# Optimization experiments

Measured on AMD Instinct MI355X. Metric: run time of the kernel, lower is better.

## Reference

```python
import jax, jax.numpy as jnp
import numpy as np

B, D_IN, H1, H2, LAT, K = 32768, 512, 256, 128, 64, 2048
BN_EPS = 1e-5
COMMIT = 0.25


def _linear_w(k, i, o):
    # xavier-uniform-ish init
    lim = np.sqrt(6.0 / (i + o)).astype(np.float32)
    return jax.random.uniform(k, (i, o), jnp.float32, -lim, lim)


def _bn_params(keys, n):
    g = jax.random.uniform(keys[0], (n,), jnp.float32, 0.5, 1.5)
    b = 0.1 * jax.random.normal(keys[1], (n,), jnp.float32)
    m = 0.1 * jax.random.normal(keys[2], (n,), jnp.float32)
    v = jax.random.uniform(keys[3], (n,), jnp.float32, 0.5, 1.5)
    return g, b, m, v


def setup_inputs() -> dict:
    key = jax.random.key(0)
    ks = jax.random.split(key, 32)
    inp = {"x": jax.random.normal(ks[0], (B, D_IN), jnp.float32)}
    # encoder: 512 -> 256 -> 128 -> 64
    inp["ew1"], inp["eb1"] = _linear_w(ks[1], D_IN, H1), jnp.zeros((H1,), jnp.float32)
    inp["eg1"], inp["ebt1"], inp["em1"], inp["ev1"] = _bn_params(jax.random.split(ks[2], 4), H1)
    inp["ew2"], inp["eb2"] = _linear_w(ks[3], H1, H2), jnp.zeros((H2,), jnp.float32)
    inp["eg2"], inp["ebt2"], inp["em2"], inp["ev2"] = _bn_params(jax.random.split(ks[4], 4), H2)
    inp["ew3"], inp["eb3"] = _linear_w(ks[5], H2, LAT), jnp.zeros((LAT,), jnp.float32)
    # codebook (num_embeddings, latent_dim)
    inp["codebook"] = _linear_w(ks[6], K, LAT).reshape(K, LAT)
    # decoder: 64 -> 128 -> 256 -> 512
    inp["dw1"], inp["db1"] = _linear_w(ks[7], LAT, H2), jnp.zeros((H2,), jnp.float32)
    inp["dg1"], inp["dbt1"], inp["dm1"], inp["dv1"] = _bn_params(jax.random.split(ks[8], 4), H2)
    inp["dw2"], inp["db2"] = _linear_w(ks[9], H2, H1), jnp.zeros((H1,), jnp.float32)
    inp["dg2"], inp["dbt2"], inp["dm2"], inp["dv2"] = _bn_params(jax.random.split(ks[10], 4), H1)
    inp["dw3"], inp["db3"] = _linear_w(ks[11], H1, D_IN), jnp.zeros((D_IN,), jnp.float32)
    return inp


def _bn(x, g, b, m, v):
    # BatchNorm1d in eval mode: running stats
    return (x - m) * (g * jax.lax.rsqrt(v + BN_EPS)) + b


def reference(x, ew1, eb1, eg1, ebt1, em1, ev1,
              ew2, eb2, eg2, ebt2, em2, ev2,
              ew3, eb3, codebook,
              dw1, db1, dg1, dbt1, dm1, dv1,
              dw2, db2, dg2, dbt2, dm2, dv2,
              dw3, db3):
    # ---- encoder MLP (Dropout is identity in eval) ----
    h = _bn(jax.nn.relu(x @ ew1 + eb1), eg1, ebt1, em1, ev1)
    h = _bn(jax.nn.relu(h @ ew2 + eb2), eg2, ebt2, em2, ev2)
    z_e = h @ ew3 + eb3  # [B, LAT]

    # ---- vector quantization: cdist + argmin + gather ----
    # squared L2 distance (argmin-equivalent to cdist p=2)
    d2 = (jnp.sum(z_e * z_e, axis=1, keepdims=True)
          + jnp.sum(codebook * codebook, axis=1)[None, :]
          - 2.0 * (z_e @ codebook.T))  # [B, K]
    idx = jnp.argmin(d2, axis=-1)  # [B]
    z_q = codebook[idx]  # gather, [B, LAT]

    codebook_loss = jnp.mean((z_q - jax.lax.stop_gradient(z_e)) ** 2)
    commit_loss = jnp.mean((z_e - jax.lax.stop_gradient(z_q)) ** 2)
    vq_loss = codebook_loss + COMMIT * commit_loss

    # straight-through estimator
    z_q = z_e + jax.lax.stop_gradient(z_q - z_e)

    # ---- decoder MLP ----
    h = _bn(jax.nn.relu(z_q @ dw1 + db1), dg1, dbt1, dm1, dv1)
    h = _bn(jax.nn.relu(h @ dw2 + db2), dg2, dbt2, dm2, dv2)
    x_recon = h @ dw3 + db3  # [B, D_IN]

    recon_err = jnp.mean((x_recon - x) ** 2)
    return x_recon, vq_loss, idx, recon_err
```

## Files before the change

### kernel.cpp

```cpp
#include <hip/hip_runtime.h>

#define B_ROWS 32768
#define D_IN   512
#define H1_N   256
#define H2_N   128
#define LAT_N  64
#define K_CB   2048

#define VQ_MARGIN 6.0e-3f
#define BK 32
#define BN 128

typedef __attribute__((ext_vector_type(8))) short s8v;
typedef __attribute__((ext_vector_type(4))) float f4v;

__device__ inline unsigned short f2bf(float f) {
    union { float f; unsigned u; } v; v.f = f;
    unsigned r = v.u + 0x7fffu + ((v.u >> 16) & 1u);
    return (unsigned short)(r >> 16);
}
__device__ inline float bf2f(unsigned short h) {
    union { unsigned u; float f; } v; v.u = ((unsigned)h) << 16;
    return v.f;
}

__device__ inline int pidx(int r, int k, int K) {
    return ((r >> 4) * (K >> 5) + (k >> 5)) * 512 + (((k >> 3) & 3) << 7)
         + ((r & 15) << 3) + (k & 7);
}

#define SWZ(row) ((((row) >> 2) & 7) << 3)

template <int MODE, int K, int CT, bool ASPLIT>
__global__ __launch_bounds__(256, 2) void mfma_gemm(
    const float* __restrict__ A_f32,
    const unsigned short* __restrict__ A_hi,
    const unsigned short* __restrict__ A_lo,
    const unsigned short* __restrict__ w_hi,
    const unsigned short* __restrict__ w_lo,
    const float* __restrict__ bias,
    const float* __restrict__ bn_g, const float* __restrict__ bn_b,
    const float* __restrict__ bn_m, const float* __restrict__ bn_v,
    unsigned short* __restrict__ out_hi, unsigned short* __restrict__ out_lo,
    float* __restrict__ out_f32,
    const float* __restrict__ xref, float* __restrict__ partials, int N)
{
    const int lane = threadIdx.x & 63;
    const int wv = threadIdx.x >> 6;
    const int wr = wv >> 1, wc = wv & 1;
    const int rbase = blockIdx.x * 128 + wr * 64;
    const int cbase = blockIdx.y * (32 * CT) + wc * (16 * CT);
    const int lr = lane & 15, lg = lane >> 4;

    f4v acc[4][CT];
#pragma unroll
    for (int rt = 0; rt < 4; ++rt)
#pragma unroll
        for (int ct = 0; ct < CT; ++ct)
            acc[rt][ct] = (f4v){0.f, 0.f, 0.f, 0.f};

    for (int ks = 0; ks < K / 32; ++ks) {
        s8v ah[4], al[4], bh[CT], bl[CT];
#pragma unroll
        for (int rt = 0; rt < 4; ++rt) {
            if constexpr (ASPLIT) {
                size_t aoff = (size_t)(rbase + rt * 16 + lr) * K + ks * 32 + lg * 8;
                const float* p = &A_f32[aoff];
                float4 v0 = *reinterpret_cast<const float4*>(p);
                float4 v1 = *reinterpret_cast<const float4*>(p + 4);
                float fv[8] = {v0.x, v0.y, v0.z, v0.w, v1.x, v1.y, v1.z, v1.w};
                unsigned uu[8], llv[8];
#pragma unroll
                for (int j = 0; j < 8; ++j) {
                    uu[j] = __float_as_uint(fv[j]);
                    float lo = fv[j] - __uint_as_float(uu[j] & 0xffff0000u);
                    llv[j] = __float_as_uint(lo);
                }
                union { s8v v; unsigned w[4]; } H, L;
#pragma unroll
                for (int m = 0; m < 4; ++m) {
                    H.w[m] = __builtin_amdgcn_perm(uu[2 * m + 1], uu[2 * m], 0x07060302u);
                    L.w[m] = __builtin_amdgcn_perm(llv[2 * m + 1], llv[2 * m], 0x07060302u);
                }
                ah[rt] = H.v;
                al[rt] = L.v;
            } else {
                int off = (((rbase >> 4) + rt) * (K >> 5) + ks) * 512 + lg * 128 + lr * 8;
                ah[rt] = *reinterpret_cast<const s8v*>(&A_hi[off]);
                al[rt] = *reinterpret_cast<const s8v*>(&A_lo[off]);
            }
        }
#pragma unroll
        for (int ct = 0; ct < CT; ++ct) {
            int off = (((cbase >> 4) + ct) * (K >> 5) + ks) * 512 + lg * 128 + lr * 8;
            bh[ct] = *reinterpret_cast<const s8v*>(&w_hi[off]);
            bl[ct] = *reinterpret_cast<const s8v*>(&w_lo[off]);
        }
#pragma unroll
        for (int rt = 0; rt < 4; ++rt)
#pragma unroll
            for (int ct = 0; ct < CT; ++ct) {
                acc[rt][ct] = __builtin_amdgcn_mfma_f32_16x16x32_bf16(
                    ah[rt], bh[ct], acc[rt][ct], 0, 0, 0);
                acc[rt][ct] = __builtin_amdgcn_mfma_f32_16x16x32_bf16(
                    al[rt], bh[ct], acc[rt][ct], 0, 0, 0);
                acc[rt][ct] = __builtin_amdgcn_mfma_f32_16x16x32_bf16(
                    ah[rt], bl[ct], acc[rt][ct], 0, 0, 0);
            }
    }

    float sq = 0.f;
#pragma unroll
    for (int ct = 0; ct < CT; ++ct) {
        int col = cbase + ct * 16 + lr;
        float bi = bias[col];
        float sc = 0.f, sh = 0.f;
        if (MODE == 0) {
            float s = bn_g[col] * rsqrtf(bn_v[col] + 1e-5f);
            sc = s;
            sh = bn_b[col] - bn_m[col] * s;
        }
#pragma unroll
        for (int rt = 0; rt < 4; ++rt)
#pragma unroll
            for (int i = 0; i < 4; ++i) {
                int row = rbase + rt * 16 + lg * 4 + i;
                float v = acc[rt][ct][i] + bi;
                if (MODE == 0) v = fmaxf(v, 0.f) * sc + sh;
                if (MODE == 0 || MODE == 3) {
                    unsigned u = __float_as_uint(v);
                    int p = pidx(row, col, N);
                    out_hi[p] = (unsigned short)(u >> 16);
                    out_lo[p] = f2bf(v - __uint_as_float(u & 0xffff0000u));
                }
                if (MODE == 2) {
                    float d = v - xref[(size_t)row * N + col];
                    sq = fmaf(d, d, sq);
                }
                if (MODE == 2 || MODE == 3)
                    out_f32[(size_t)row * N + col] = v;
            }
    }
    if (MODE == 2) {
        __shared__ float red[256];
        red[threadIdx.x] = sq;
        __syncthreads();
        for (int off = 128; off > 0; off >>= 1) {
            if (threadIdx.x < off) red[threadIdx.x] += red[threadIdx.x + off];
            __syncthreads();
        }
        if (threadIdx.x == 0)
            partials[blockIdx.y * gridDim.x + blockIdx.x] = red[0];
    }
}

template <int MODE, bool GATHER>
__global__ __launch_bounds__(256, 6) void rgemm(
    const int* __restrict__ rcnt, const int* __restrict__ rlist,
    const float* __restrict__ A, const float* __restrict__ W,
    const float* __restrict__ bias,
    const float* __restrict__ bn_g, const float* __restrict__ bn_b,
    const float* __restrict__ bn_m, const float* __restrict__ bn_v,
    float* __restrict__ out, int M, int N)
{
    const int count = min(rcnt[0], B_ROWS);
    const int row0 = blockIdx.x * 64;
    if (row0 >= count) return;
    __shared__ float sA[BK][64];
    __shared__ float sB[BK][BN];
    const int tid = threadIdx.x;
    const int tr = tid >> 4;
    const int tc = tid & 15;
    const int n0 = blockIdx.y * BN;

    float acc[4][8];
#pragma unroll
    for (int i = 0; i < 4; ++i)
#pragma unroll
        for (int j = 0; j < 8; ++j) acc[i][j] = 0.f;

    for (int k0 = 0; k0 < M; k0 += BK) {
#pragma unroll
        for (int it = 0; it < 2; ++it) {
            int s = tid + it * 256;
            int m = s >> 3;
            int kq = s & 7;
            int i = row0 + m;
            int src;
            if (GATHER) {
                int rr = (i < count) ? rlist[i] : 0;
                src = ((unsigned)rr < (unsigned)B_ROWS) ? rr : 0;
            } else {
                src = i;
            }
            float4 v = *reinterpret_cast<const float4*>(
                &A[(size_t)src * M + k0 + kq * 4]);
            int kk = kq * 4;
            sA[kk + 0][m ^ SWZ(kk + 0)] = v.x;
            sA[kk + 1][m ^ SWZ(kk + 1)] = v.y;
            sA[kk + 2][m ^ SWZ(kk + 2)] = v.z;
            sA[kk + 3][m ^ SWZ(kk + 3)] = v.w;
        }
#pragma unroll
        for (int it = 0; it < 4; ++it) {
            int s = tid + it * 256;
            int k = s >> 5;
            int nq = s & 31;
            int n = n0 + nq * 4;
            float4 v = make_float4(0.f, 0.f, 0.f, 0.f);
            if (n < N)
                v = *reinterpret_cast<const float4*>(&W[(size_t)(k0 + k) * N + n]);
            *reinterpret_cast<float4*>(&sB[k][nq * 4]) = v;
        }
        __syncthreads();
#pragma unroll 4
        for (int k = 0; k < BK; ++k) {
            int ac = (tr * 4) ^ SWZ(k);
            float4 a0 = *reinterpret_cast<float4*>(&sA[k][ac]);
            float a[4] = {a0.x, a0.y, a0.z, a0.w};
            float4 b0 = *reinterpret_cast<float4*>(&sB[k][tc * 4]);
            float4 b1 = *reinterpret_cast<float4*>(&sB[k][64 + tc * 4]);
            float b[8] = {b0.x, b0.y, b0.z, b0.w, b1.x, b1.y, b1.z, b1.w};
#pragma unroll
            for (int i = 0; i < 4; ++i)
#pragma unroll
                for (int j = 0; j < 8; ++j)
                    acc[i][j] = fmaf(a[i], b[j], acc[i][j]);
        }
        __syncthreads();
    }

    const int nb0 = n0 + tc * 4;
    const int nb1 = n0 + 64 + tc * 4;
    float bi[8], sc[8], sh[8];
#pragma unroll
    for (int g = 0; g < 2; ++g) {
        int nb = g ? nb1 : nb0;
        if (nb < N) {
#pragma unroll
            for (int j = 0; j < 4; ++j) {
                int n = nb + j;
                bi[g * 4 + j] = bias[n];
                if (MODE == 0) {
                    float s = bn_g[n] * rsqrtf(bn_v[n] + 1e-5f);
                    sc[g * 4 + j] = s;
                    sh[g * 4 + j] = bn_b[n] - bn_m[n] * s;
                }
            }
        }
    }
#pragma unroll
    for (int i = 0; i < 4; ++i) {
        int row = row0 + tr * 4 + i;
#pragma unroll
        for (int g = 0; g < 2; ++g) {
            int nb = g ? nb1 : nb0;
            if (nb < N) {
                float o[4];
#pragma unroll
                for (int j = 0; j < 4; ++j) {
                    float v = acc[i][g * 4 + j] + bi[g * 4 + j];
                    if (MODE == 0) {
                        v = v > 0.f ? v : 0.f;
                        v = v * sc[g * 4 + j] + sh[g * 4 + j];
                    }
                    o[j] = v;
                }
                *reinterpret_cast<float4*>(&out[(size_t)row * N + nb]) =
                    make_float4(o[0], o[1], o[2], o[3]);
            }
        }
    }
}

__device__ inline void wprep_packed(const float* __restrict__ w,
                                    unsigned short* __restrict__ w_hi,
                                    unsigned short* __restrict__ w_lo,
                                    int K, int N, int t)
{
    if (t >= N * (K >> 3)) return;
    int n = t / (K >> 3);
    int k0 = (t - n * (K >> 3)) << 3;
    union { unsigned short s[8]; uint4 v; } H, L;
#pragma unroll
    for (int j = 0; j < 8; ++j) {
        float f = w[(size_t)(k0 + j) * N + n];
        unsigned u = __float_as_uint(f);
        float lo = f - __uint_as_float(u & 0xffff0000u);
        H.s[j] = (unsigned short)(u >> 16);
        L.s[j] = f2bf(lo);
    }
    int p = pidx(n, k0, K);
    *reinterpret_cast<uint4*>(&w_hi[p]) = H.v;
    *reinterpret_cast<uint4*>(&w_lo[p]) = L.v;
}

__global__ __launch_bounds__(256) void prep_all(
    const float* __restrict__ dw3, unsigned short* w3hi, unsigned short* w3lo,
    const float* __restrict__ dw2, unsigned short* w2hi, unsigned short* w2lo,
    const float* __restrict__ dw1, unsigned short* w1hi, unsigned short* w1lo,
    const float* __restrict__ ew1, unsigned short* e1hi, unsigned short* e1lo,
    const float* __restrict__ ew2, unsigned short* e2hi, unsigned short* e2lo,
    const float* __restrict__ ew3, unsigned short* e3hi, unsigned short* e3lo,
    const float* __restrict__ cb, unsigned short* cb_hi, unsigned short* cb_lo,
    float* __restrict__ cn, int* __restrict__ rcnt, float* __restrict__ repairp)
{
    int bid = blockIdx.x;
    int tid = threadIdx.x;
    if (bid < 64) {
        wprep_packed(dw3, w3hi, w3lo, H1_N, D_IN, bid * 256 + tid);
    } else if (bid < 80) {
        wprep_packed(dw2, w2hi, w2lo, H2_N, H1_N, (bid - 64) * 256 + tid);
    } else if (bid < 84) {
        wprep_packed(dw1, w1hi, w1lo, LAT_N, H2_N, (bid - 80) * 256 + tid);
    } else if (bid < 148) {
        wprep_packed(ew1, e1hi, e1lo, D_IN, H1_N, (bid - 84) * 256 + tid);
    } else if (bid < 164) {
        wprep_packed(ew2, e2hi, e2lo, H1_N, H2_N, (bid - 148) * 256 + tid);
    } else if (bid < 168) {
        wprep_packed(ew3, e3hi, e3lo, H2_N, LAT_N, (bid - 164) * 256 + tid);
    } else {
        int blk = bid - 168;
        if (blk == 0) {
            if (tid == 0) rcnt[0] = 0;
            repairp[tid] = 0.f;
        }
        int j = blk * 256 + tid;
        float s = 0.f;
#pragma unroll
        for (int g = 0; g < 8; ++g) {
            float4 v0 = *reinterpret_cast<const float4*>(&cb[(size_t)j * LAT_N + g * 8]);
            float4 v1 = *reinterpret_cast<const float4*>(&cb[(size_t)j * LAT_N + g * 8 + 4]);
            float e[8] = {v0.x, v0.y, v0.z, v0.w, v1.x, v1.y, v1.z, v1.w};
            union { unsigned short us[8]; uint4 v; } H, L;
#pragma unroll
            for (int t = 0; t < 8; ++t) {
                s = fmaf(e[t], e[t], s);
                unsigned short hb = f2bf(e[t]);
                H.us[t] = hb;
                L.us[t] = f2bf(e[t] - bf2f(hb));
            }
            int p = pidx(j, g * 8, LAT_N);
            *reinterpret_cast<uint4*>(&cb_hi[p]) = H.v;
            *reinterpret_cast<uint4*>(&cb_lo[p]) = L.v;
        }
        cn[j] = s;
    }
}

__global__ __launch_bounds__(256) void vq_mfma(
    const unsigned short* __restrict__ zhi, const unsigned short* __restrict__ zlo,
    const unsigned short* __restrict__ cb_hi,
    const unsigned short* __restrict__ cb_lo, const float* __restrict__ cnorm,
    float4* __restrict__ cand)
{
    const int lane = threadIdx.x & 63;
    const int wid  = blockIdx.x * 4 + (threadIdx.x >> 6);
    const int rbase = (wid >> 3) * 64;
    const int cblk  = wid & 7;
    const int cbase = cblk * 256;
    const int lr = lane & 15;
    const int lg = lane >> 4;

    s8v a_hi[4][2], a_lo[4][2];
#pragma unroll
    for (int rt = 0; rt < 4; ++rt) {
#pragma unroll
        for (int ks = 0; ks < 2; ++ks) {
            int off = (((rbase >> 4) + rt) * 2 + ks) * 512 + lg * 128 + lr * 8;
            a_hi[rt][ks] = *reinterpret_cast<const s8v*>(&zhi[off]);
            a_lo[rt][ks] = *reinterpret_cast<const s8v*>(&zlo[off]);
        }
    }

    float b1[4][4], b2[4][4];
    int j1[4][4];
#pragma unroll
    for (int rt = 0; rt < 4; ++rt)
#pragma unroll
        for (int i = 0; i < 4; ++i) {
            b1[rt][i] = 3.4e38f; b2[rt][i] = 3.4e38f; j1[rt][i] = 0;
        }

    for (int ct = 0; ct < 16; ++ct) {
        int col = cbase + ct * 16 + lr;
        int t0 = (((cbase >> 4) + ct) * 2 + 0) * 512 + lg * 128 + lr * 8;
        int t1 = t0 + 512;
        s8v bh0 = *reinterpret_cast<const s8v*>(&cb_hi[t0]);
        s8v bh1 = *reinterpret_cast<const s8v*>(&cb_hi[t1]);
        s8v bl0 = *reinterpret_cast<const s8v*>(&cb_lo[t0]);
        s8v bl1 = *reinterpret_cast<const s8v*>(&cb_lo[t1]);
        float cn = cnorm[col];
#pragma unroll
        for (int rt = 0; rt < 4; ++rt) {
            f4v acc = {0.f, 0.f, 0.f, 0.f};
            acc = __builtin_amdgcn_mfma_f32_16x16x32_bf16(a_hi[rt][0], bh0, acc, 0, 0, 0);
            acc = __builtin_amdgcn_mfma_f32_16x16x32_bf16(a_hi[rt][1], bh1, acc, 0, 0, 0);
            acc = __builtin_amdgcn_mfma_f32_16x16x32_bf16(a_lo[rt][0], bh0, acc, 0, 0, 0);
            acc = __builtin_amdgcn_mfma_f32_16x16x32_bf16(a_lo[rt][1], bh1, acc, 0, 0, 0);
            acc = __builtin_amdgcn_mfma_f32_16x16x32_bf16(a_hi[rt][0], bl0, acc, 0, 0, 0);
            acc = __builtin_amdgcn_mfma_f32_16x16x32_bf16(a_hi[rt][1], bl1, acc, 0, 0, 0);
#pragma unroll
            for (int i = 0; i < 4; ++i) {
                float d = fmaf(-2.f, acc[i], cn);
                if (d < b1[rt][i]) {
                    b2[rt][i] = b1[rt][i];
                    b1[rt][i] = d;
                    j1[rt][i] = col;
                } else if (d < b2[rt][i]) {
                    b2[rt][i] = d;
                }
            }
        }
    }

#pragma unroll
    for (int off = 1; off < 16; off <<= 1) {
#pragma unroll
        for (int rt = 0; rt < 4; ++rt)
#pragma unroll
            for (int i = 0; i < 4; ++i) {
                float o1 = __shfl_xor(b1[rt][i], off);
                float o2 = __shfl_xor(b2[rt][i], off);
                int oj = __shfl_xor(j1[rt][i], off);
                float nb2 = fminf(fmaxf(b1[rt][i], o1), fminf(b2[rt][i], o2));
                if (o1 < b1[rt][i] ||
                    (o1 == b1[rt][i] && oj < j1[rt][i])) {
                    b1[rt][i] = o1;
                    j1[rt][i] = oj;
                }
                b2[rt][i] = nb2;
            }
    }
    if (lr == 0) {
#pragma unroll
        for (int rt = 0; rt < 4; ++rt)
#pragma unroll
            for (int i = 0; i < 4; ++i) {
                int row = rbase + rt * 16 + lg * 4 + i;
                cand[(size_t)row * 8 + cblk] = make_float4(
                    b1[rt][i], __int_as_float(j1[rt][i]), b2[rt][i], 0.f);
            }
    }
}

__global__ __launch_bounds__(256) void vq_merge(
    const float4* __restrict__ cand, const float* __restrict__ z,
    const float* __restrict__ cb,
    const unsigned short* __restrict__ cbhi,
    const unsigned short* __restrict__ cblo,
    unsigned short* __restrict__ zqhi, unsigned short* __restrict__ zqlo,
    float* __restrict__ idxf,
    int* __restrict__ rlist, int* __restrict__ rcnt,
    float* __restrict__ mergep)
{
    __shared__ float red[256];
    int tid = threadIdx.x;
    int row = blockIdx.x * 256 + tid;
    const float4* c = &cand[(size_t)row * 8];
    float4 c0 = c[0];
    float b1 = c0.x, b2 = c0.z;
    int j1 = __float_as_int(c0.y);
#pragma unroll
    for (int t = 1; t < 8; ++t) {
        float4 ct = c[t];
        float o1 = ct.x, o2 = ct.z;
        int oj = __float_as_int(ct.y);
        float nb2 = fminf(fmaxf(b1, o1), fminf(b2, o2));
        if (o1 < b1 || (o1 == b1 && oj < j1)) { b1 = o1; j1 = oj; }
        b2 = nb2;
    }
    idxf[row] = (float)j1;
    float sq = 0.f;
    if (b2 - b1 >= VQ_MARGIN) {
#pragma unroll
        for (int lq = 0; lq < 16; ++lq) {
            float4 cv = *reinterpret_cast<const float4*>(&cb[(size_t)j1 * LAT_N + lq * 4]);
            float4 zv = *reinterpret_cast<const float4*>(&z[(size_t)row * LAT_N + lq * 4]);
            float d0 = cv.x - zv.x, d1 = cv.y - zv.y;
            float d2 = cv.z - zv.z, d3 = cv.w - zv.w;
            sq = fmaf(d0, d0, sq); sq = fmaf(d1, d1, sq);
            sq = fmaf(d2, d2, sq); sq = fmaf(d3, d3, sq);
        }
#pragma unroll
        for (int g = 0; g < 8; ++g) {
            int sp = pidx(j1, g * 8, LAT_N);
            int dp = pidx(row, g * 8, LAT_N);
            *reinterpret_cast<uint4*>(&zqhi[dp]) =
                *reinterpret_cast<const uint4*>(&cbhi[sp]);
            *reinterpret_cast<uint4*>(&zqlo[dp]) =
                *reinterpret_cast<const uint4*>(&cblo[sp]);
        }
    } else {
        int s = atomicAdd(rcnt, 1);
        if (s < B_ROWS) rlist[s] = row;
    }
    red[tid] = sq;
    __syncthreads();
    for (int off = 128; off > 0; off >>= 1) {
        if (tid < off) red[tid] += red[tid + off];
        __syncthreads();
    }
    if (tid == 0) mergep[blockIdx.x] = red[0];
}

#define RB 8
__global__ __launch_bounds__(256) void repair_scan(
    const int* __restrict__ rcnt, const int* __restrict__ rlist,
    const float* __restrict__ zr,
    const float* __restrict__ cb, const float* __restrict__ cn,
    const unsigned short* __restrict__ cbhi,
    const unsigned short* __restrict__ cblo,
    unsigned short* __restrict__ zqhi, unsigned short* __restrict__ zqlo,
    float* __restrict__ idxf, float* __restrict__ repairp)
{
    __shared__ float sz[RB][LAT_N];
    __shared__ float rv[256];
    __shared__ int ri[256];
    const int tid = threadIdx.x;
    const int count = min(rcnt[0], B_ROWS);
    if (blockIdx.x * RB >= count) return;
    float lsum = 0.f;
    for (int base = blockIdx.x * RB; base < count; base += gridDim.x * RB) {
        int nr = min(RB, count - base);
        __syncthreads();
        for (int s = tid; s < nr * LAT_N; s += 256) {
            int r = s >> 6, d = s & 63;
            sz[r][d] = zr[(size_t)(base + r) * LAT_N + d];
        }
        __syncthreads();
        float bv[RB];
        int bj[RB];
#pragma unroll
        for (int r = 0; r < RB; ++r) { bv[r] = 3.4e38f; bj[r] = 0; }
        for (int k = 0; k < K_CB / 256; ++k) {
            int cidx = tid + k * 256;
            float a[RB];
#pragma unroll
            for (int r = 0; r < RB; ++r) a[r] = 0.f;
            const float* cp = &cb[(size_t)cidx * LAT_N];
#pragma unroll 2
            for (int d4 = 0; d4 < 16; ++d4) {
                float4 cv = *reinterpret_cast<const float4*>(cp + d4 * 4);
#pragma unroll
                for (int r = 0; r < RB; ++r) {
                    a[r] = fmaf(sz[r][d4 * 4 + 0], cv.x, a[r]);
                    a[r] = fmaf(sz[r][d4 * 4 + 1], cv.y, a[r]);
                    a[r] = fmaf(sz[r][d4 * 4 + 2], cv.z, a[r]);
                    a[r] = fmaf(sz[r][d4 * 4 + 3], cv.w, a[r]);
                }
            }
            float cnv = cn[cidx];
#pragma unroll
            for (int r = 0; r < RB; ++r) {
                float d = fmaf(-2.f, a[r], cnv);
                if (d < bv[r] || (d == bv[r] && cidx < bj[r])) {
                    bv[r] = d; bj[r] = cidx;
                }
            }
        }
        for (int r = 0; r < RB; ++r) {
            if (r >= nr) break;
            rv[tid] = bv[r];
            ri[tid] = bj[r];
            __syncthreads();
            for (int off = 128; off > 0; off >>= 1) {
                if (tid < off) {
                    float ov = rv[tid + off];
                    int oi = ri[tid + off];
                    if (ov < rv[tid] || (ov == rv[tid] && oi < ri[tid])) {
                        rv[tid] = ov; ri[tid] = oi;
                    }
                }
                __syncthreads();
            }
            int bjf = ri[0];
            int rr = rlist[base + r];
            bool ok = (unsigned)rr < (unsigned)B_ROWS;
            rr = ok ? rr : 0;
            if (tid == 0 && ok) idxf[rr] = (float)bjf;
            float v = 0.f;
            if (tid < 64) {
                float d = cb[(size_t)bjf * LAT_N + tid] - sz[r][tid];
                v = d * d;
            }
            __syncthreads();
            rv[tid] = v;
            __syncthreads();
            for (int off = 128; off > 0; off >>= 1) {
                if (tid < off) rv[tid] += rv[tid + off];
                __syncthreads();
            }
            if (tid == 0) lsum += rv[0];
            if (ok) {
                if (tid < 8) {
                    int g = tid;
                    *reinterpret_cast<uint4*>(&zqhi[pidx(rr, g * 8, LAT_N)]) =
                        *reinterpret_cast<const uint4*>(&cbhi[pidx(bjf, g * 8, LAT_N)]);
                } else if (tid < 16) {
                    int g = tid - 8;
                    *reinterpret_cast<uint4*>(&zqlo[pidx(rr, g * 8, LAT_N)]) =
                        *reinterpret_cast<const uint4*>(&cblo[pidx(bjf, g * 8, LAT_N)]);
                }
            }
            __syncthreads();
        }
    }
    if (tid == 0) repairp[blockIdx.x] = lsum;
}

__global__ __launch_bounds__(256) void finalize_kernel(
    const float* __restrict__ mergep, int nm,
    const float* __restrict__ repairp, int nr,
    const float* __restrict__ rep, int nre,
    float* __restrict__ vq_out, float* __restrict__ re_out)
{
    __shared__ float s[256];
    int tid = threadIdx.x;
    float a = 0.f;
    for (int i = tid; i < nm; i += 256) a += mergep[i];
    for (int i = tid; i < nr; i += 256) a += repairp[i];
    s[tid] = a;
    __syncthreads();
    for (int off = 128; off > 0; off >>= 1) {
        if (tid < off) s[tid] += s[tid + off];
        __syncthreads();
    }
    if (tid == 0) *vq_out = 1.25f * s[0] / (float)(B_ROWS * LAT_N);
    __syncthreads();
    float b = 0.f;
    for (int i = tid; i < nre; i += 256) b += rep[i];
    s[tid] = b;
    __syncthreads();
    for (int off = 128; off > 0; off >>= 1) {
        if (tid < off) s[tid] += s[tid + off];
        __syncthreads();
    }
    if (tid == 0) *re_out = s[0] / (float)(B_ROWS * D_IN);
}

extern "C" void kernel_launch(void* const* d_in, const int* in_sizes, int n_in,
                              void* d_out, int out_size, void* d_ws, size_t ws_size,
                              hipStream_t stream)
{
    const float* x    = (const float*)d_in[0];
    const float* ew1  = (const float*)d_in[1];
    const float* eb1  = (const float*)d_in[2];
    const float* eg1  = (const float*)d_in[3];
    const float* ebt1 = (const float*)d_in[4];
    const float* em1  = (const float*)d_in[5];
    const float* ev1  = (const float*)d_in[6];
    const float* ew2  = (const float*)d_in[7];
    const float* eb2  = (const float*)d_in[8];
    const float* eg2  = (const float*)d_in[9];
    const float* ebt2 = (const float*)d_in[10];
    const float* em2  = (const float*)d_in[11];
    const float* ev2  = (const float*)d_in[12];
    const float* ew3  = (const float*)d_in[13];
    const float* eb3  = (const float*)d_in[14];
    const float* cb   = (const float*)d_in[15];
    const float* dw1  = (const float*)d_in[16];
    const float* db1  = (const float*)d_in[17];
    const float* dg1  = (const float*)d_in[18];
    const float* dbt1 = (const float*)d_in[19];
    const float* dm1  = (const float*)d_in[20];
    const float* dv1  = (const float*)d_in[21];
    const float* dw2  = (const float*)d_in[22];
    const float* db2  = (const float*)d_in[23];
    const float* dg2  = (const float*)d_in[24];
    const float* dbt2 = (const float*)d_in[25];
    const float* dm2  = (const float*)d_in[26];
    const float* dv2  = (const float*)d_in[27];
    const float* dw3  = (const float*)d_in[28];
    const float* db3  = (const float*)d_in[29];

    float* outf = (float*)d_out;
    const size_t XR_OFF = 0;
    const size_t VQ_OFF = (size_t)B_ROWS * D_IN;
    const size_t IDX_OFF = VQ_OFF + 1;
    const size_t RE_OFF = IDX_OFF + B_ROWS;

    float* wsf = (float*)d_ws;
    size_t off = 0;
    float* buf256 = wsf + off; off += (size_t)B_ROWS * H1_N;
    float* buf128 = wsf + off; off += (size_t)B_ROWS * H2_N;
    float* zbuf   = wsf + off; off += (size_t)B_ROWS * LAT_N;
    float* zr     = wsf + off; off += (size_t)B_ROWS * LAT_N;
    float* cnbuf  = wsf + off; off += K_CB;
    float* mergep = wsf + off; off += 128;
    float* repairp= wsf + off; off += 256;
    float* rep    = wsf + off; off += 1024;
    unsigned short* cbhi = (unsigned short*)(wsf + off); off += K_CB * LAT_N / 2;
    unsigned short* cblo = (unsigned short*)(wsf + off); off += K_CB * LAT_N / 2;
    float4* candb = (float4*)(wsf + off); off += (size_t)B_ROWS * 8 * 4;
    int* rcnt  = (int*)(wsf + off); off += 16;
    int* rlist = (int*)(wsf + off); off += B_ROWS;
    unsigned short* w1hi = (unsigned short*)(wsf + off); off += (H2_N * LAT_N) / 2;
    unsigned short* w1lo = (unsigned short*)(wsf + off); off += (H2_N * LAT_N) / 2;
    unsigned short* w2hi = (unsigned short*)(wsf + off); off += (H1_N * H2_N) / 2;
    unsigned short* w2lo = (unsigned short*)(wsf + off); off += (H1_N * H2_N) / 2;
    unsigned short* w3hi = (unsigned short*)(wsf + off); off += (D_IN * H1_N) / 2;
    unsigned short* w3lo = (unsigned short*)(wsf + off); off += (D_IN * H1_N) / 2;
    unsigned short* e1hi = (unsigned short*)(wsf + off); off += (D_IN * H1_N) / 2;
    unsigned short* e1lo = (unsigned short*)(wsf + off); off += (D_IN * H1_N) / 2;
    unsigned short* e2hi = (unsigned short*)(wsf + off); off += (H1_N * H2_N) / 2;
    unsigned short* e2lo = (unsigned short*)(wsf + off); off += (H1_N * H2_N) / 2;
    unsigned short* e3hi = (unsigned short*)(wsf + off); off += (H2_N * LAT_N) / 2;
    unsigned short* e3lo = (unsigned short*)(wsf + off); off += (H2_N * LAT_N) / 2;
    unsigned short* zqhi = (unsigned short*)(wsf + off); off += (size_t)B_ROWS * LAT_N / 2;
    unsigned short* zqlo = (unsigned short*)(wsf + off); off += (size_t)B_ROWS * LAT_N / 2;

    unsigned short* eh1hi = (unsigned short*)buf256;
    unsigned short* eh1lo = (unsigned short*)(buf256 + (size_t)B_ROWS * 128);
    unsigned short* zhi   = (unsigned short*)buf256;
    unsigned short* zlo   = (unsigned short*)(buf256 + (size_t)B_ROWS * 32);
    float*          h1r   = buf256;
    unsigned short* dh2hi = (unsigned short*)buf256;
    unsigned short* dh2lo = (unsigned short*)(buf256 + (size_t)B_ROWS * 128);
    unsigned short* eh2hi = (unsigned short*)buf128;
    unsigned short* eh2lo = (unsigned short*)(buf128 + (size_t)B_ROWS * 64);
    float*          h2r   = buf128;
    unsigned short* dh1hi = (unsigned short*)buf128;
    unsigned short* dh1lo = (unsigned short*)(buf128 + (size_t)B_ROWS * 64);

    dim3 blk(256);
    const int GXM = B_ROWS / 128;
    const int GM64 = B_ROWS / 64;

    prep_all<<<dim3(176), blk, 0, stream>>>(
        dw3, w3hi, w3lo, dw2, w2hi, w2lo, dw1, w1hi, w1lo,
        ew1, e1hi, e1lo, ew2, e2hi, e2lo, ew3, e3hi, e3lo,
        cb, cbhi, cblo, cnbuf, rcnt, repairp);

    mfma_gemm<0, D_IN, 4, true><<<dim3(GXM, H1_N / 128), blk, 0, stream>>>(
        x, nullptr, nullptr, e1hi, e1lo, eb1, eg1, ebt1, em1, ev1,
        eh1hi, eh1lo, nullptr, nullptr, nullptr, H1_N);
    mfma_gemm<0, H1_N, 4, false><<<dim3(GXM, 1), blk, 0, stream>>>(
        nullptr, eh1hi, eh1lo, e2hi, e2lo, eb2, eg2, ebt2, em2, ev2,
        eh2hi, eh2lo, nullptr, nullptr, nullptr, H2_N);
    mfma_gemm<3, H2_N, 2, false><<<dim3(GXM, 1), blk, 0, stream>>>(
        nullptr, eh2hi, eh2lo, e3hi, e3lo, eb3, nullptr, nullptr, nullptr, nullptr,
        zhi, zlo, zbuf, nullptr, nullptr, LAT_N);

    vq_mfma<<<dim3(1024), blk, 0, stream>>>(zhi, zlo, cbhi, cblo, cnbuf, candb);
    vq_merge<<<dim3(B_ROWS / 256), blk, 0, stream>>>(
        candb, zbuf, cb, cbhi, cblo, zqhi, zqlo,
        outf + IDX_OFF, rlist, rcnt, mergep);

    rgemm<0, true><<<dim3(GM64, 2), blk, 0, stream>>>(
        rcnt, rlist, x, ew1, eb1, eg1, ebt1, em1, ev1, h1r, D_IN, H1_N);
    rgemm<0, false><<<dim3(GM64, 1), blk, 0, stream>>>(
        rcnt, rlist, h1r, ew2, eb2, eg2, ebt2, em2, ev2, h2r, H1_N, H2_N);
    rgemm<1, false><<<dim3(GM64, 1), blk, 0, stream>>>(
        rcnt, rlist, h2r, ew3, eb3, nullptr, nullptr, nullptr, nullptr,
        zr, H2_N, LAT_N);
    repair_scan<<<dim3(256), blk, 0, stream>>>(
        rcnt, rlist, zr, cb, cnbuf, cbhi, cblo, zqhi, zqlo,
        outf + IDX_OFF, repairp);

    mfma_gemm<0, LAT_N, 4, false><<<dim3(GXM, 1), blk, 0, stream>>>(
        nullptr, zqhi, zqlo, w1hi, w1lo, db1, dg1, dbt1, dm1, dv1,
        dh1hi, dh1lo, nullptr, nullptr, nullptr, H2_N);
    mfma_gemm<0, H2_N, 4, false><<<dim3(GXM, H1_N / 128), blk, 0, stream>>>(
        nullptr, dh1hi, dh1lo, w2hi, w2lo, db2, dg2, dbt2, dm2, dv2,
        dh2hi, dh2lo, nullptr, nullptr, nullptr, H1_N);
    mfma_gemm<2, H1_N, 4, false><<<dim3(GXM, D_IN / 128), blk, 0, stream>>>(
        nullptr, dh2hi, dh2lo, w3hi, w3lo, db3, nullptr, nullptr, nullptr, nullptr,
        nullptr, nullptr, outf + XR_OFF, x, rep, D_IN);

    finalize_kernel<<<dim3(1), blk, 0, stream>>>(
        mergep, 128, repairp, 256, rep, 1024, outf + VQ_OFF, outf + RE_OFF);
}
```

Baseline: 434.7 us.

## Pre-split x into packed bf16 hi/lo and double-buffer GEMM fragment loads

Adds an xsplit kernel that converts x once into bf16 hi/lo parts stored in the packed MFMA layout, so the first encoder GEMM no longer recomputes the split in its inner loop for each column block. The mfma_gemm K loop is rewritten with two register fragment sets (A/B), loading the next k-step while MFMAs run on the current one, to hide global-load latency. The cost is an extra kernel launch, 64 MB of extra workspace traffic for the split x, and higher register pressure from doubled fragments. That pressure could cause spills under launch_bounds(256,2).

```diff
diff --git a/kernel.cpp b/kernel.cpp
--- a/kernel.cpp
+++ b/kernel.cpp
@@ -31,9 +31,32 @@
 
 #define SWZ(row) ((((row) >> 2) & 7) << 3)
 
-template <int MODE, int K, int CT, bool ASPLIT>
+__global__ __launch_bounds__(256) void xsplit(
+    const float* __restrict__ x, unsigned short* __restrict__ xhi,
+    unsigned short* __restrict__ xlo)
+{
+    int t = blockIdx.x * 256 + threadIdx.x;
+    int r = t >> 6;
+    int g = t & 63;
+    const float* p = &x[(size_t)r * D_IN + g * 8];
+    float4 v0 = *reinterpret_cast<const float4*>(p);
+    float4 v1 = *reinterpret_cast<const float4*>(p + 4);
+    float fv[8] = {v0.x, v0.y, v0.z, v0.w, v1.x, v1.y, v1.z, v1.w};
+    union { unsigned short s[8]; uint4 v; } H, L;
+#pragma unroll
+    for (int j = 0; j < 8; ++j) {
+        unsigned u = __float_as_uint(fv[j]);
+        float lo = fv[j] - __uint_as_float(u & 0xffff0000u);
+        H.s[j] = (unsigned short)(u >> 16);
+        L.s[j] = f2bf(lo);
+    }
+    int pp = pidx(r, g * 8, D_IN);
+    *reinterpret_cast<uint4*>(&xhi[pp]) = H.v;
+    *reinterpret_cast<uint4*>(&xlo[pp]) = L.v;
+}
+
+template <int MODE, int K, int CT>
 __global__ __launch_bounds__(256, 2) void mfma_gemm(
-    const float* __restrict__ A_f32,
     const unsigned short* __restrict__ A_hi,
     const unsigned short* __restrict__ A_lo,
     const unsigned short* __restrict__ w_hi,
@@ -45,12 +68,14 @@
     float* __restrict__ out_f32,
     const float* __restrict__ xref, float* __restrict__ partials, int N)
 {
+    constexpr int NK = K / 32;
     const int lane = threadIdx.x & 63;
     const int wv = threadIdx.x >> 6;
     const int wr = wv >> 1, wc = wv & 1;
     const int rbase = blockIdx.x * 128 + wr * 64;
     const int cbase = blockIdx.y * (32 * CT) + wc * (16 * CT);
     const int lr = lane & 15, lg = lane >> 4;
+    const int lofs = lg * 128 + lr * 8;
 
     f4v acc[4][CT];
 #pragma unroll
@@ -59,55 +84,50 @@
         for (int ct = 0; ct < CT; ++ct)
             acc[rt][ct] = (f4v){0.f, 0.f, 0.f, 0.f};
 
-    for (int ks = 0; ks < K / 32; ++ks) {
-        s8v ah[4], al[4], bh[CT], bl[CT];
-#pragma unroll
-        for (int rt = 0; rt < 4; ++rt) {
-            if constexpr (ASPLIT) {
-                size_t aoff = (size_t)(rbase + rt * 16 + lr) * K + ks * 32 + lg * 8;
-                const float* p = &A_f32[aoff];
-                float4 v0 = *reinterpret_cast<const float4*>(p);
-                float4 v1 = *reinterpret_cast<const float4*>(p + 4);
-                float fv[8] = {v0.x, v0.y, v0.z, v0.w, v1.x, v1.y, v1.z, v1.w};
-                unsigned uu[8], llv[8];
-#pragma unroll
-                for (int j = 0; j < 8; ++j) {
-                    uu[j] = __float_as_uint(fv[j]);
-                    float lo = fv[j] - __uint_as_float(uu[j] & 0xffff0000u);
-                    llv[j] = __float_as_uint(lo);
-                }
-                union { s8v v; unsigned w[4]; } H, L;
-#pragma unroll
-                for (int m = 0; m < 4; ++m) {
-                    H.w[m] = __builtin_amdgcn_perm(uu[2 * m + 1], uu[2 * m], 0x07060302u);
-                    L.w[m] = __builtin_amdgcn_perm(llv[2 * m + 1], llv[2 * m], 0x07060302u);
-                }
-                ah[rt] = H.v;
-                al[rt] = L.v;
-            } else {
-                int off = (((rbase >> 4) + rt) * (K >> 5) + ks) * 512 + lg * 128 + lr * 8;
-                ah[rt] = *reinterpret_cast<const s8v*>(&A_hi[off]);
-                al[rt] = *reinterpret_cast<const s8v*>(&A_lo[off]);
-            }
-        }
-#pragma unroll
-        for (int ct = 0; ct < CT; ++ct) {
-            int off = (((cbase >> 4) + ct) * (K >> 5) + ks) * 512 + lg * 128 + lr * 8;
-            bh[ct] = *reinterpret_cast<const s8v*>(&w_hi[off]);
-            bl[ct] = *reinterpret_cast<const s8v*>(&w_lo[off]);
-        }
-#pragma unroll
-        for (int rt = 0; rt < 4; ++rt)
-#pragma unroll
-            for (int ct = 0; ct < CT; ++ct) {
-                acc[rt][ct] = __builtin_amdgcn_mfma_f32_16x16x32_bf16(
-                    ah[rt], bh[ct], acc[rt][ct], 0, 0, 0);
-                acc[rt][ct] = __builtin_amdgcn_mfma_f32_16x16x32_bf16(
-                    al[rt], bh[ct], acc[rt][ct], 0, 0, 0);
-                acc[rt][ct] = __builtin_amdgcn_mfma_f32_16x16x32_bf16(
-                    ah[rt], bl[ct], acc[rt][ct], 0, 0, 0);
-            }
-    }
+    s8v ahA[4], alA[4], bhA[CT], blA[CT];
+    s8v ahB[4], alB[4], bhB[CT], blB[CT];
+
+#define LOADF(S, KS)                                                          \
+    {                                                                         \
+        _Pragma("unroll")                                                     \
+        for (int rt = 0; rt < 4; ++rt) {                                      \
+            int aoff = (((rbase >> 4) + rt) * NK + (KS)) * 512 + lofs;        \
+            ah##S[rt] = *reinterpret_cast<const s8v*>(&A_hi[aoff]);           \
+            al##S[rt] = *reinterpret_cast<const s8v*>(&A_lo[aoff]);           \
+        }                                                                     \
+        _Pragma("unroll")                                                     \
+        for (int ct = 0; ct < CT; ++ct) {                                     \
+            int woff = (((cbase >> 4) + ct) * NK + (KS)) * 512 + lofs;        \
+            bh##S[ct] = *reinterpret_cast<const s8v*>(&w_hi[woff]);           \
+            bl##S[ct] = *reinterpret_cast<const s8v*>(&w_lo[woff]);           \
+        }                                                                     \
+    }
+
+#define MFMAF(S)                                                              \
+    {                                                                         \
+        _Pragma("unroll")                                                     \
+        for (int rt = 0; rt < 4; ++rt)                                        \
+            _Pragma("unroll")                                                 \
+            for (int ct = 0; ct < CT; ++ct) {                                 \
+                acc[rt][ct] = __builtin_amdgcn_mfma_f32_16x16x32_bf16(        \
+                    ah##S[rt], bh##S[ct], acc[rt][ct], 0, 0, 0);              \
+                acc[rt][ct] = __builtin_amdgcn_mfma_f32_16x16x32_bf16(        \
+                    al##S[rt], bh##S[ct], acc[rt][ct], 0, 0, 0);              \
+                acc[rt][ct] = __builtin_amdgcn_mfma_f32_16x16x32_bf16(        \
+                    ah##S[rt], bl##S[ct], acc[rt][ct], 0, 0, 0);              \
+            }                                                                 \
+    }
+
+    LOADF(A, 0);
+#pragma unroll
+    for (int k2 = 0; k2 < NK / 2; ++k2) {
+        LOADF(B, 2 * k2 + 1);
+        MFMAF(A);
+        if (k2 + 1 < NK / 2) LOADF(A, 2 * k2 + 2);
+        MFMAF(B);
+    }
+#undef LOADF
+#undef MFMAF
 
     float sq = 0.f;
 #pragma unroll
@@ -709,6 +729,8 @@
     unsigned short* e3lo = (unsigned short*)(wsf + off); off += (H2_N * LAT_N) / 2;
     unsigned short* zqhi = (unsigned short*)(wsf + off); off += (size_t)B_ROWS * LAT_N / 2;
     unsigned short* zqlo = (unsigned short*)(wsf + off); off += (size_t)B_ROWS * LAT_N / 2;
+    unsigned short* xhi  = (unsigned short*)(wsf + off); off += (size_t)B_ROWS * D_IN / 2;
+    unsigned short* xlo  = (unsigned short*)(wsf + off); off += (size_t)B_ROWS * D_IN / 2;
 
     unsigned short* eh1hi = (unsigned short*)buf256;
     unsigned short* eh1lo = (unsigned short*)(buf256 + (size_t)B_ROWS * 128);
@@ -731,15 +753,16 @@
         dw3, w3hi, w3lo, dw2, w2hi, w2lo, dw1, w1hi, w1lo,
         ew1, e1hi, e1lo, ew2, e2hi, e2lo, ew3, e3hi, e3lo,
         cb, cbhi, cblo, cnbuf, rcnt, repairp);
-
-    mfma_gemm<0, D_IN, 4, true><<<dim3(GXM, H1_N / 128), blk, 0, stream>>>(
-        x, nullptr, nullptr, e1hi, e1lo, eb1, eg1, ebt1, em1, ev1,
+    xsplit<<<dim3(B_ROWS * (D_IN / 8) / 256), blk, 0, stream>>>(x, xhi, xlo);
+
+    mfma_gemm<0, D_IN, 4><<<dim3(GXM, H1_N / 128), blk, 0, stream>>>(
+        xhi, xlo, e1hi, e1lo, eb1, eg1, ebt1, em1, ev1,
         eh1hi, eh1lo, nullptr, nullptr, nullptr, H1_N);
-    mfma_gemm<0, H1_N, 4, false><<<dim3(GXM, 1), blk, 0, stream>>>(
-        nullptr, eh1hi, eh1lo, e2hi, e2lo, eb2, eg2, ebt2, em2, ev2,
+    mfma_gemm<0, H1_N, 4><<<dim3(GXM, 1), blk, 0, stream>>>(
+        eh1hi, eh1lo, e2hi, e2lo, eb2, eg2, ebt2, em2, ev2,
         eh2hi, eh2lo, nullptr, nullptr, nullptr, H2_N);
-    mfma_gemm<3, H2_N, 2, false><<<dim3(GXM, 1), blk, 0, stream>>>(
-        nullptr, eh2hi, eh2lo, e3hi, e3lo, eb3, nullptr, nullptr, nullptr, nullptr,
+    mfma_gemm<3, H2_N, 2><<<dim3(GXM, 1), blk, 0, stream>>>(
+        eh2hi, eh2lo, e3hi, e3lo, eb3, nullptr, nullptr, nullptr, nullptr,
         zhi, zlo, zbuf, nullptr, nullptr, LAT_N);
 
     vq_mfma<<<dim3(1024), blk, 0, stream>>>(zhi, zlo, cbhi, cblo, cnbuf, candb);
@@ -758,14 +781,14 @@
         rcnt, rlist, zr, cb, cnbuf, cbhi, cblo, zqhi, zqlo,
         outf + IDX_OFF, repairp);
 
-    mfma_gemm<0, LAT_N, 4, false><<<dim3(GXM, 1), blk, 0, stream>>>(
-        nullptr, zqhi, zqlo, w1hi, w1lo, db1, dg1, dbt1, dm1, dv1,
+    mfma_gemm<0, LAT_N, 4><<<dim3(GXM, 1), blk, 0, stream>>>(
+        zqhi, zqlo, w1hi, w1lo, db1, dg1, dbt1, dm1, dv1,
         dh1hi, dh1lo, nullptr, nullptr, nullptr, H2_N);
-    mfma_gemm<0, H2_N, 4, false><<<dim3(GXM, H1_N / 128), blk, 0, stream>>>(
-        nullptr, dh1hi, dh1lo, w2hi, w2lo, db2, dg2, dbt2, dm2, dv2,
+    mfma_gemm<0, H2_N, 4><<<dim3(GXM, H1_N / 128), blk, 0, stream>>>(
+        dh1hi, dh1lo, w2hi, w2lo, db2, dg2, dbt2, dm2, dv2,
         dh2hi, dh2lo, nullptr, nullptr, nullptr, H1_N);
-    mfma_gemm<2, H1_N, 4, false><<<dim3(GXM, D_IN / 128), blk, 0, stream>>>(
-        nullptr, dh2hi, dh2lo, w3hi, w3lo, db3, nullptr, nullptr, nullptr, nullptr,
+    mfma_gemm<2, H1_N, 4><<<dim3(GXM, D_IN / 128), blk, 0, stream>>>(
+        dh2hi, dh2lo, w3hi, w3lo, db3, nullptr, nullptr, nullptr, nullptr,
         nullptr, nullptr, outf + XR_OFF, x, rep, D_IN);
 
     finalize_kernel<<<dim3(1), blk, 0, stream>>>(
```

Result: slower. 470.4 us (+8.2%).
